# Optimization experiments

Measured on AMD Instinct MI355X. Metric: run time of the kernel, lower is better.

Reference implementation:

```python
import math
import jax, jax.numpy as jnp
import numpy as np

# Module config (init_kwargs)
GRID = (11, 16, 24)          # (T, H, W) latent grid, T odd so T-1 == 2*(T//2)
POOL = 128                   # pool_size / block size
SPARSITY = 0.9
TXT_LEN = 384                # txt_len, txt_first=False
HEADS, HDIM = 8, 128
FFL = GRID[1] * GRID[2]      # first_frame_len = H*W = 384
SEQ = GRID[0] * FFL + TXT_LEN  # 4608 tokens, 36 blocks of 128


def _rearr(t):
    # rearrange_with_remaining, h%8==0 and w%8==0 path.
    # t: [b, (f h w), n, d] with f = T-1 frames (first frame excluded)
    b, s, n, d = t.shape
    T, H, W = GRID
    fn, hn, wn = T // 2, H // 8, W // 8
    x = t.transpose(0, 2, 1, 3).reshape(b * n, fn, 2, hn, 8, wn, 8, d)
    # 'b (fn fb)(hn hb)(wn wb) d -> b (fn hn wn fb hb wb) d'
    x = x.transpose(0, 1, 3, 5, 2, 4, 6, 7).reshape(b * n, s, d)
    return x.reshape(b, n, s, d).transpose(0, 2, 1, 3)


def _inv_rearr(t):
    b, s, n, d = t.shape
    T, H, W = GRID
    fn, hn, wn = T // 2, H // 8, W // 8
    x = t.transpose(0, 2, 1, 3).reshape(b * n, fn, hn, wn, 2, 8, 8, d)
    x = x.transpose(0, 1, 4, 2, 5, 3, 6, 7).reshape(b * n, s, d)
    return x.reshape(b, n, s, d).transpose(0, 2, 1, 3)


def _avgpool(t):
    # seq divisible by POOL -> mean over each block (tail branch unused)
    b, s, n, d = t.shape
    return t.reshape(b, s // POOL, POOL, n, d).mean(axis=2)


def _forward(q, k, v):
    b, s, n, d = q.shape
    scale = jnp.asarray(d, q.dtype) ** -0.5
    # do_tensor_rearrange_pooling on concatenated qkv (txt_first=False)
    qkv = jnp.concatenate([q, k, v], axis=0)
    f_part = qkv[:, :FFL]
    i_part = qkv[:, FFL:s - TXT_LEN]
    t_part = qkv[:, s - TXT_LEN:]
    qkv2 = jnp.concatenate([_rearr(i_part), f_part, t_part], axis=1)
    pool = _avgpool(qkv2)
    q2, k2, v2 = jnp.split(qkv2, 3, axis=0)
    qp, kp, _ = jnp.split(pool, 3, axis=0)
    # pooled block scores + softmax
    ps = jax.nn.softmax(jnp.einsum('blnd,bsnd->bnls', qp, kp) * scale, axis=-1)
    nb = s // POOL
    keep = math.ceil(nb * (1.0 - SPARSITY))
    thr = jax.lax.top_k(ps, keep)[0][..., -1:]
    mask = ps >= thr                              # [B, n, nb, nb] bool
    prot = (FFL + TXT_LEN + POOL - 1) // POOL
    mask = mask.at[:, :, -prot:, :].set(True)
    mask = mask.at[:, :, :, -prot:].set(True)
    bm = mask[0]                                  # [n, nb, nb] per-head block mask (batch 0, as kernel uses)
    tok = jnp.repeat(jnp.repeat(bm, POOL, axis=1), POOL, axis=2)  # [n, S, S]
    # block-sparse attention == masked dense attention over selected kv blocks
    scores = jnp.einsum('bqnd,bknd->bnqk', q2, k2) * scale
    scores = jnp.where(tok[None], scores, jnp.asarray(-1e30, scores.dtype))
    p = jax.nn.softmax(scores, axis=-1)
    x = jnp.einsum('bnqk,bknd->bqnd', p, v2)
    # do_tensor_inv_rearrange (txt_first=False: concat(f, i, t))
    si = s - TXT_LEN - FFL
    xi = _inv_rearr(x[:, :si])
    xf = x[:, si:si + FFL]
    xt = x[:, si + FFL:]
    return jnp.concatenate([xf, xi, xt], axis=1)


def setup_inputs() -> dict:
    key = jax.random.key(0)
    kq, kk, kv = jax.random.split(key, 3)
    q = jax.random.normal(kq, (1, SEQ, HEADS, HDIM), dtype=jnp.float32)
    k = jax.random.normal(kk, (1, SEQ, HEADS, HDIM), dtype=jnp.float32)
    v = jax.random.normal(kv, (1, SEQ, HEADS, HDIM), dtype=jnp.float32)
    t_b_idx = jnp.arange(2, dtype=jnp.int64 if jax.config.jax_enable_x64 else jnp.int32)
    return {'q': q, 'k': k, 'v': v, 't_b_idx': t_b_idx}


def reference(q, k, v, t_b_idx):
    # t_idx = t_b_idx[0] = 0, skip_timesteps = 0 -> sparse branch (static)
    return _forward(q, k, v)
```

## Files before the change

kernel.cpp:

```cpp
#include <hip/hip_runtime.h>


typedef __attribute__((ext_vector_type(8))) _Float16 half8;
typedef __attribute__((ext_vector_type(4))) _Float16 half4;
typedef __attribute__((ext_vector_type(4))) float float4v;

#define KROW 136
#define VROW 72
#define PROW 72

__device__ __forceinline__ int orig_pos(int j) {
    if (j >= 3840) return (j < 4224) ? (j - 3840) : j;
    int blk = j >> 7;
    int r   = j & 127;
    int f   = blk / 6;
    int rem = blk - f * 6;
    int b2  = rem / 3;
    int e   = rem - b2 * 3;
    int a   = r >> 6;
    int c   = (r >> 3) & 7;
    int g   = r & 7;
    return 384 + (f * 2 + a) * 384 + (b2 * 8 + c) * 24 + e * 8 + g;
}

__device__ __forceinline__ void cp16(const void* g, void* l) {
    __builtin_amdgcn_global_load_lds((const __attribute__((address_space(1))) void*)g,
                                     (__attribute__((address_space(3))) void*)l, 16, 0, 0);
}

__global__ __launch_bounds__(256) void prep_kernel(const float* __restrict__ q,
                                                   const float* __restrict__ k,
                                                   const float* __restrict__ v,
                                                   short* __restrict__ Kc,
                                                   unsigned* __restrict__ Vt32,
                                                   float* __restrict__ qp,
                                                   float* __restrict__ kp) {
    __shared__ short Vs[64 * KROW];
    __shared__ float Rs[8 * 128];
    int bx  = blockIdx.x;
    int tid = threadIdx.x;
    int sub = bx & 1;
    int kb  = (bx >> 1) % 36;
    int h   = bx / 72;

    {
        int lr = tid >> 3;
        int ld = (tid & 7) << 2;
#pragma unroll
        for (int pass = 0; pass < 2; ++pass) {
            int lt  = pass * 32 + lr;
            int tok = sub * 64 + lt;
            int op  = orig_pos(kb * 128 + tok);
            const float* kr = k + ((size_t)op * 8 + h) * 128;
            const float* vr = v + ((size_t)op * 8 + h) * 128;
            short* ko = Kc + ((size_t)(h * 36 + kb) * 128 + tok) * KROW;
#pragma unroll
            for (int j = 0; j < 4; ++j) {
                int d = ld + j * 32;
                float4v xk = *reinterpret_cast<const float4v*>(kr + d);
                float4v xv = *reinterpret_cast<const float4v*>(vr + d);
                half4 hk, hv;
#pragma unroll
                for (int i = 0; i < 4; ++i) { hk[i] = (_Float16)xk[i]; hv[i] = (_Float16)xv[i]; }
                *reinterpret_cast<half4*>(ko + d) = hk;
                *reinterpret_cast<half4*>(&Vs[lt * KROW + d]) = hv;
            }
        }
    }

    {
        const float* arr = sub ? q : k;
        int dq = (tid & 31) << 2;
        int g  = tid >> 5;
        float4v acc = {0.f, 0.f, 0.f, 0.f};
        for (int t = g; t < 128; t += 8) {
            int op = orig_pos(kb * 128 + t);
            float4v x = *reinterpret_cast<const float4v*>(arr + ((size_t)op * 8 + h) * 128 + dq);
            acc[0] += x[0]; acc[1] += x[1]; acc[2] += x[2]; acc[3] += x[3];
        }
#pragma unroll
        for (int i = 0; i < 4; ++i) Rs[g * 128 + dq + i] = acc[i];
    }
    __syncthreads();

    {
        const unsigned short* Vsu = (const unsigned short*)Vs;
        unsigned* vo = Vt32 + (size_t)((h * 36 + kb) * 2 + sub) * 128 * (VROW / 2);
#pragma unroll
        for (int it = 0; it < 16; ++it) {
            int i   = it * 256 + tid;
            int tw  = i & 31;
            int dim = i >> 5;
            unsigned lo = Vsu[(2 * tw) * KROW + dim];
            unsigned hi = Vsu[(2 * tw + 1) * KROW + dim];
            vo[dim * (VROW / 2) + tw] = (hi << 16) | lo;
        }
    }

    if (tid < 128) {
        float s = 0.f;
#pragma unroll
        for (int g = 0; g < 8; ++g) s += Rs[g * 128 + tid];
        float* outp = sub ? qp : kp;
        outp[(h * 36 + kb) * 128 + tid] = s * (1.f / 128.f);
    }
}

__global__ __launch_bounds__(256, 3) void flash_kernel(const float* __restrict__ q,
                                                       const short* __restrict__ Kc,
                                                       const short* __restrict__ Vt,
                                                       const float* __restrict__ qp,
                                                       const float* __restrict__ kp,
                                                       float* __restrict__ out,
                                                       float* __restrict__ pO,
                                                       float* __restrict__ pL) {
    __shared__ __align__(16) short Ks[64 * KROW];
    __shared__ __align__(16) short Vsh[128 * VROW];
    __shared__ __align__(16) short Ph[4 * 16 * PROW];
    __shared__ int Ls[40];

    int t = blockIdx.x;
    int h, qb, half, nkb = 0, kbase = 0, pidx = -1;
    if (t < 288) {
        h = t & 7;
        int rest = t >> 3;
        int qbh = rest / 6, r2 = rest % 6;
        half = r2 / 3;
        int chunk = r2 % 3;
        qb = 30 + qbh; nkb = 12; kbase = chunk * 12; pidx = t;
    } else {
        int t2 = t - 288;
        h = t2 & 7;
        int rest = t2 >> 3;
        qb = rest >> 1; half = rest & 1;
    }

    int tid = threadIdx.x, wave = tid >> 6, lane = tid & 63;
    int m16 = lane & 15, quad = lane >> 4;

    int qrow_frag = qb * 128 + half * 64 + wave * 16 + m16;
    const float* qrp = q + ((size_t)orig_pos(qrow_frag) * 8 + h) * 128;
    half8 aq[4];
#pragma unroll
    for (int kc = 0; kc < 4; ++kc) {
        float4v x0 = *reinterpret_cast<const float4v*>(qrp + kc * 32 + quad * 8);
        float4v x1 = *reinterpret_cast<const float4v*>(qrp + kc * 32 + quad * 8 + 4);
#pragma unroll
        for (int j = 0; j < 4; ++j) { aq[kc][j] = (_Float16)x0[j]; aq[kc][4 + j] = (_Float16)x1[j]; }
    }

    if (pidx < 0 && wave == 0) {
        float s = -1e30f;
        if (lane < 36) {
            const float4v* qv = (const float4v*)(qp + (h * 36 + qb) * 128);
            const float4v* kv = (const float4v*)(kp + (h * 36 + lane) * 128);
            float acc = 0.f;
            for (int i = 0; i < 32; ++i) {
                float4v a = qv[i], b = kv[i];
                acc += a[0] * b[0] + a[1] * b[1] + a[2] * b[2] + a[3] * b[3];
            }
            s = acc;
        }
        float tmp = s;
        float thr = 0.f;
        for (int i = 0; i < 4; ++i) {
            float mx = tmp;
            for (int off = 1; off < 64; off <<= 1) mx = fmaxf(mx, __shfl_xor(mx, off));
            thr = mx;
            unsigned long long bal = __ballot(tmp == mx);
            int low = __ffsll(bal) - 1;
            if (lane == low) tmp = -3e38f;
        }
        bool keep = (lane < 36) && ((s >= thr) || (lane >= 30));
        unsigned long long mk = __ballot(keep);
        if (lane == 0) Ls[0] = __popcll(mk);
        if (keep) {
            int pos = __popcll(mk & ((1ull << lane) - 1ull));
            Ls[1 + pos] = lane;
        }
    }
    __syncthreads();
    if (pidx < 0) nkb = Ls[0];

    float l_r[4], o[8][4];
#pragma unroll
    for (int r = 0; r < 4; ++r) l_r[r] = 0.f;
#pragma unroll
    for (int dt = 0; dt < 8; ++dt)
#pragma unroll
        for (int r = 0; r < 4; ++r) o[dt][r] = 0.f;

    constexpr float kScale = 0.08838834764831845f * 1.4426950408889634f;
    short* Phw = Ph + wave * (16 * PROW);

    int ntile = nkb * 2;
    for (int it = 0; it < ntile; ++it) {
        int kb  = (pidx >= 0) ? (kbase + (it >> 1)) : Ls[1 + (it >> 1)];
        int sub = it & 1;
        const char* gK = (const char*)(Kc + ((size_t)((h * 36 + kb) * 128) + sub * 64) * KROW);
        const char* gV = (const char*)(Vt + (size_t)((h * 36 + kb) * 2 + sub) * 128 * VROW);

        __syncthreads();
        {
            char* lK = (char*)Ks;
            char* lV = (char*)Vsh;
            int off = lane * 16;
            for (int c = wave; c < 35; c += 4) {
                if (c < 17) cp16(gK + c * 1024 + off, lK + c * 1024 + off);
                else        cp16(gV + (c - 17) * 1024 + off, lV + (c - 17) * 1024 + off);
            }
        }
        __syncthreads();

        float4v sacc[4];
#pragma unroll
        for (int nt = 0; nt < 4; ++nt) { sacc[nt][0] = 0.f; sacc[nt][1] = 0.f; sacc[nt][2] = 0.f; sacc[nt][3] = 0.f; }
#pragma unroll
        for (int nt = 0; nt < 4; ++nt)
#pragma unroll
            for (int kc = 0; kc < 4; ++kc) {
                half8 bk = *reinterpret_cast<const half8*>(&Ks[(nt * 16 + m16) * KROW + kc * 32 + quad * 8]);
                sacc[nt] = __builtin_amdgcn_mfma_f32_16x16x32_f16(aq[kc], bk, sacc[nt], 0, 0, 0);
            }

#pragma unroll
        for (int r = 0; r < 4; ++r) {
            float p0 = exp2f(sacc[0][r] * kScale);
            float p1 = exp2f(sacc[1][r] * kScale);
            float p2 = exp2f(sacc[2][r] * kScale);
            float p3 = exp2f(sacc[3][r] * kScale);
            sacc[0][r] = p0; sacc[1][r] = p1; sacc[2][r] = p2; sacc[3][r] = p3;
            l_r[r] += (p0 + p1) + (p2 + p3);
        }

#pragma unroll
        for (int nt = 0; nt < 4; ++nt)
#pragma unroll
            for (int r = 0; r < 4; ++r) {
                union { _Float16 hf; short s; } cv;
                cv.hf = (_Float16)sacc[nt][r];
                Phw[(quad * 4 + r) * PROW + nt * 16 + m16] = cv.s;
            }
        half8 ap0 = *reinterpret_cast<const half8*>(&Phw[m16 * PROW + quad * 8]);
        half8 ap1 = *reinterpret_cast<const half8*>(&Phw[m16 * PROW + 32 + quad * 8]);

#pragma unroll
        for (int dt = 0; dt < 8; ++dt) {
            float4v oc;
            oc[0] = o[dt][0]; oc[1] = o[dt][1]; oc[2] = o[dt][2]; oc[3] = o[dt][3];
            half8 bv0 = *reinterpret_cast<const half8*>(&Vsh[(dt * 16 + m16) * VROW + quad * 8]);
            half8 bv1 = *reinterpret_cast<const half8*>(&Vsh[(dt * 16 + m16) * VROW + 32 + quad * 8]);
            oc = __builtin_amdgcn_mfma_f32_16x16x32_f16(ap0, bv0, oc, 0, 0, 0);
            oc = __builtin_amdgcn_mfma_f32_16x16x32_f16(ap1, bv1, oc, 0, 0, 0);
            o[dt][0] = oc[0]; o[dt][1] = oc[1]; o[dt][2] = oc[2]; o[dt][3] = oc[3];
        }
    }

#pragma unroll
    for (int r = 0; r < 4; ++r)
        for (int sh = 1; sh < 16; sh <<= 1) l_r[r] += __shfl_xor(l_r[r], sh);

    if (pidx >= 0) {
        float* po = pO + (size_t)pidx * 8192;
#pragma unroll
        for (int r = 0; r < 4; ++r) {
            int row = wave * 16 + quad * 4 + r;
#pragma unroll
            for (int dt = 0; dt < 8; ++dt)
                po[row * 128 + dt * 16 + m16] = o[dt][r];
            if (m16 == 0) pL[pidx * 64 + row] = l_r[r];
        }
    } else {
#pragma unroll
        for (int r = 0; r < 4; ++r) {
            int qrow = qb * 128 + half * 64 + wave * 16 + quad * 4 + r;
            size_t base = ((size_t)orig_pos(qrow) * 8 + h) * 128;
            float inv = 1.f / l_r[r];
#pragma unroll
            for (int dt = 0; dt < 8; ++dt)
                out[base + dt * 16 + m16] = o[dt][r] * inv;
        }
    }
}

__global__ void combine_kernel(const float* __restrict__ pO, const float* __restrict__ pL,
                               float* __restrict__ out) {
    int g = blockIdx.x;
    int h    = g / 12;
    int rem  = g % 12;
    int qbh  = rem >> 1;
    int half = rem & 1;
    int qb   = 30 + qbh;
    int base_t = (qbh * 6 + half * 3) * 8 + h;

    int tid = threadIdx.x;
    int d   = tid & 127;
    int r0  = tid >> 7;
    for (int itr = 0; itr < 32; ++itr) {
        int row = r0 + itr * 2;
        float l = pL[(base_t + 0) * 64 + row] + pL[(base_t + 8) * 64 + row] + pL[(base_t + 16) * 64 + row];
        float acc = pO[(size_t)(base_t + 0) * 8192 + row * 128 + d]
                  + pO[(size_t)(base_t + 8) * 8192 + row * 128 + d]
                  + pO[(size_t)(base_t + 16) * 8192 + row * 128 + d];
        int qrow = qb * 128 + half * 64 + row;
        out[((size_t)orig_pos(qrow) * 8 + h) * 128 + d] = acc / l;
    }
}

extern "C" void kernel_launch(void* const* d_in, const int* in_sizes, int n_in,
                              void* d_out, int out_size, void* d_ws, size_t ws_size,
                              hipStream_t stream) {
    const float* q = (const float*)d_in[0];
    const float* k = (const float*)d_in[1];
    const float* v = (const float*)d_in[2];
    float* out = (float*)d_out;

    char* w = (char*)d_ws;
    short* Kc  = (short*)(w);
    short* Vt  = (short*)(w + 10027008);
    float* qp  = (float*)(w + 20643840);
    float* kp  = (float*)(w + 20791296);
    float* pL  = (float*)(w + 20938752);
    float* pO  = (float*)(w + 21012480);

    prep_kernel<<<dim3(576), dim3(256), 0, stream>>>(q, k, v, Kc, (unsigned*)Vt, qp, kp);
    flash_kernel<<<dim3(768), dim3(256), 0, stream>>>(q, Kc, Vt, qp, kp, out, pO, pL);
    combine_kernel<<<dim3(96), dim3(256), 0, stream>>>(pO, pL, out);
}
```

Measured before the change: 192.0 us.

## Double-buffer K/V tiles in LDS with async prefetch and parallelize combine

The flash kernel now keeps two LDS buffers for K and V and prefetches the tile two steps ahead with async global-to-LDS copies. Explicit vmcnt waits and barriers replace the old load-then-sync at each step, so tile loads overlap with the MFMA work. The V row pitch shrinks to 68 so the doubled buffers fit, MFMA sections get raised wave priority, and launch bounds drop to two blocks per CU. The combine kernel is split across eight times as many blocks. The costs are lower occupancy, V rows that are no longer 16-byte aligned, which may split LDS vector reads, and a redundant duplicate K-chunk copy added to keep the vmcnt counts uniform across waves.

```diff
diff --git a/kernel.cpp b/kernel.cpp
--- a/kernel.cpp
+++ b/kernel.cpp
@@ -6,7 +6,7 @@
 typedef __attribute__((ext_vector_type(4))) float float4v;
 
 #define KROW 136
-#define VROW 72
+#define VROW 68
 #define PROW 72
 
 __device__ __forceinline__ int orig_pos(int j) {
@@ -106,7 +106,22 @@
     }
 }
 
-__global__ __launch_bounds__(256, 3) void flash_kernel(const float* __restrict__ q,
+__device__ __forceinline__ void stage_tile(const short* __restrict__ Kc,
+                                           const short* __restrict__ Vt,
+                                           int h, int kb, int sub,
+                                           int wave, int lane,
+                                           char* lK, char* lV) {
+    const char* gK = (const char*)(Kc + ((size_t)((h * 36 + kb) * 128) + sub * 64) * KROW);
+    const char* gV = (const char*)(Vt + (size_t)((h * 36 + kb) * 2 + sub) * 128 * VROW);
+    int off = lane * 16;
+    for (int c = wave; c < 34; c += 4) {
+        if (c < 17) cp16(gK + c * 1024 + off, lK + c * 1024 + off);
+        else        cp16(gV + (c - 17) * 1024 + off, lV + (c - 17) * 1024 + off);
+    }
+    if (wave >= 2) cp16(gK + wave * 1024 + off, lK + wave * 1024 + off);
+}
+
+__global__ __launch_bounds__(256, 2) void flash_kernel(const float* __restrict__ q,
                                                        const short* __restrict__ Kc,
                                                        const short* __restrict__ Vt,
                                                        const float* __restrict__ qp,
@@ -114,8 +129,8 @@
                                                        float* __restrict__ out,
                                                        float* __restrict__ pO,
                                                        float* __restrict__ pL) {
-    __shared__ __align__(16) short Ks[64 * KROW];
-    __shared__ __align__(16) short Vsh[128 * VROW];
+    __shared__ __align__(16) short Ks[2][64 * KROW];
+    __shared__ __align__(16) short Vsh[2][128 * VROW];
     __shared__ __align__(16) short Ph[4 * 16 * PROW];
     __shared__ int Ls[40];
 
@@ -194,34 +209,32 @@
     short* Phw = Ph + wave * (16 * PROW);
 
     int ntile = nkb * 2;
+
+    {
+        int kb0 = (pidx >= 0) ? kbase : Ls[1];
+        stage_tile(Kc, Vt, h, kb0, 0, wave, lane, (char*)&Ks[0][0], (char*)&Vsh[0][0]);
+        stage_tile(Kc, Vt, h, kb0, 1, wave, lane, (char*)&Ks[1][0], (char*)&Vsh[1][0]);
+    }
+
     for (int it = 0; it < ntile; ++it) {
-        int kb  = (pidx >= 0) ? (kbase + (it >> 1)) : Ls[1 + (it >> 1)];
-        int sub = it & 1;
-        const char* gK = (const char*)(Kc + ((size_t)((h * 36 + kb) * 128) + sub * 64) * KROW);
-        const char* gV = (const char*)(Vt + (size_t)((h * 36 + kb) * 2 + sub) * 128 * VROW);
-
-        __syncthreads();
-        {
-            char* lK = (char*)Ks;
-            char* lV = (char*)Vsh;
-            int off = lane * 16;
-            for (int c = wave; c < 35; c += 4) {
-                if (c < 17) cp16(gK + c * 1024 + off, lK + c * 1024 + off);
-                else        cp16(gV + (c - 17) * 1024 + off, lV + (c - 17) * 1024 + off);
-            }
-        }
-        __syncthreads();
+        int cur = it & 1;
+        if (it + 1 < ntile) { asm volatile("s_waitcnt vmcnt(9)" ::: "memory"); }
+        else                { asm volatile("s_waitcnt vmcnt(0)" ::: "memory"); }
+        __builtin_amdgcn_s_barrier();
+        __builtin_amdgcn_sched_barrier(0);
 
         float4v sacc[4];
 #pragma unroll
         for (int nt = 0; nt < 4; ++nt) { sacc[nt][0] = 0.f; sacc[nt][1] = 0.f; sacc[nt][2] = 0.f; sacc[nt][3] = 0.f; }
+        __builtin_amdgcn_s_setprio(1);
 #pragma unroll
         for (int nt = 0; nt < 4; ++nt)
 #pragma unroll
             for (int kc = 0; kc < 4; ++kc) {
-                half8 bk = *reinterpret_cast<const half8*>(&Ks[(nt * 16 + m16) * KROW + kc * 32 + quad * 8]);
+                half8 bk = *reinterpret_cast<const half8*>(&Ks[cur][(nt * 16 + m16) * KROW + kc * 32 + quad * 8]);
                 sacc[nt] = __builtin_amdgcn_mfma_f32_16x16x32_f16(aq[kc], bk, sacc[nt], 0, 0, 0);
             }
+        __builtin_amdgcn_s_setprio(0);
 
 #pragma unroll
         for (int r = 0; r < 4; ++r) {
@@ -244,15 +257,25 @@
         half8 ap0 = *reinterpret_cast<const half8*>(&Phw[m16 * PROW + quad * 8]);
         half8 ap1 = *reinterpret_cast<const half8*>(&Phw[m16 * PROW + 32 + quad * 8]);
 
+        __builtin_amdgcn_s_setprio(1);
 #pragma unroll
         for (int dt = 0; dt < 8; ++dt) {
             float4v oc;
             oc[0] = o[dt][0]; oc[1] = o[dt][1]; oc[2] = o[dt][2]; oc[3] = o[dt][3];
-            half8 bv0 = *reinterpret_cast<const half8*>(&Vsh[(dt * 16 + m16) * VROW + quad * 8]);
-            half8 bv1 = *reinterpret_cast<const half8*>(&Vsh[(dt * 16 + m16) * VROW + 32 + quad * 8]);
+            half8 bv0 = *reinterpret_cast<const half8*>(&Vsh[cur][(dt * 16 + m16) * VROW + quad * 8]);
+            half8 bv1 = *reinterpret_cast<const half8*>(&Vsh[cur][(dt * 16 + m16) * VROW + 32 + quad * 8]);
             oc = __builtin_amdgcn_mfma_f32_16x16x32_f16(ap0, bv0, oc, 0, 0, 0);
             oc = __builtin_amdgcn_mfma_f32_16x16x32_f16(ap1, bv1, oc, 0, 0, 0);
             o[dt][0] = oc[0]; o[dt][1] = oc[1]; o[dt][2] = oc[2]; o[dt][3] = oc[3];
+        }
+        __builtin_amdgcn_s_setprio(0);
+
+        __builtin_amdgcn_sched_barrier(0);
+        __builtin_amdgcn_s_barrier();
+        if (it + 2 < ntile) {
+            int it2 = it + 2;
+            int kb2 = (pidx >= 0) ? (kbase + (it2 >> 1)) : Ls[1 + (it2 >> 1)];
+            stage_tile(Kc, Vt, h, kb2, it2 & 1, wave, lane, (char*)&Ks[cur][0], (char*)&Vsh[cur][0]);
         }
     }
 
@@ -285,7 +308,9 @@
 
 __global__ void combine_kernel(const float* __restrict__ pO, const float* __restrict__ pL,
                                float* __restrict__ out) {
-    int g = blockIdx.x;
+    int gb = blockIdx.x;
+    int g  = gb >> 3;
+    int rg = gb & 7;
     int h    = g / 12;
     int rem  = g % 12;
     int qbh  = rem >> 1;
@@ -296,8 +321,9 @@
     int tid = threadIdx.x;
     int d   = tid & 127;
     int r0  = tid >> 7;
-    for (int itr = 0; itr < 32; ++itr) {
-        int row = r0 + itr * 2;
+#pragma unroll
+    for (int itr = 0; itr < 4; ++itr) {
+        int row = rg * 8 + r0 + itr * 2;
         float l = pL[(base_t + 0) * 64 + row] + pL[(base_t + 8) * 64 + row] + pL[(base_t + 16) * 64 + row];
         float acc = pO[(size_t)(base_t + 0) * 8192 + row * 128 + d]
                   + pO[(size_t)(base_t + 8) * 8192 + row * 128 + d]
@@ -318,12 +344,12 @@
     char* w = (char*)d_ws;
     short* Kc  = (short*)(w);
     short* Vt  = (short*)(w + 10027008);
-    float* qp  = (float*)(w + 20643840);
-    float* kp  = (float*)(w + 20791296);
-    float* pL  = (float*)(w + 20938752);
-    float* pO  = (float*)(w + 21012480);
+    float* qp  = (float*)(w + 20054016);
+    float* kp  = (float*)(w + 20201472);
+    float* pL  = (float*)(w + 20348928);
+    float* pO  = (float*)(w + 20422656);
 
     prep_kernel<<<dim3(576), dim3(256), 0, stream>>>(q, k, v, Kc, (unsigned*)Vt, qp, kp);
     flash_kernel<<<dim3(768), dim3(256), 0, stream>>>(q, Kc, Vt, qp, kp, out, pO, pL);
-    combine_kernel<<<dim3(96), dim3(256), 0, stream>>>(pO, pL, out);
-}
+    combine_kernel<<<dim3(768), dim3(256), 0, stream>>>(pO, pL, out);
+}
```

New measurement: 217.7 us. 1.13x slower.

## Give each flash wave 32 query rows, split prep kernel, widen combine grid

Applied to the files above, without the earlier changes.

The flash kernel now runs 2 waves of 128 threads, each owning 32 query rows (two 16-row groups). Each K/V fragment loaded from LDS therefore feeds two MFMAs, halving LDS reads per MFMA. The softmax scale is folded into Q at load time, and the V and P LDS row padding shrinks from 72 to 68. The prep kernel is split into separate blocks for K/V conversion and for pooling, and the combine kernel uses 8 times more blocks, both to add parallelism. In exchange the flash kernel roughly doubles its accumulator registers and has fewer waves per block for latency hiding; the new padding may also change LDS bank conflicts.

```diff
diff --git a/kernel.cpp b/kernel.cpp
--- a/kernel.cpp
+++ b/kernel.cpp
@@ -6,8 +6,8 @@
 typedef __attribute__((ext_vector_type(4))) float float4v;
 
 #define KROW 136
-#define VROW 72
-#define PROW 72
+#define VROW 68
+#define PPROW 68
 
 __device__ __forceinline__ int orig_pos(int j) {
     if (j >= 3840) return (j < 4224) ? (j - 3840) : j;
@@ -39,11 +39,12 @@
     __shared__ float Rs[8 * 128];
     int bx  = blockIdx.x;
     int tid = threadIdx.x;
-    int sub = bx & 1;
-    int kb  = (bx >> 1) % 36;
-    int h   = bx / 72;
-
-    {
+
+    if (bx < 576) {
+        int sub = bx & 1;
+        int kb  = (bx >> 1) % 36;
+        int h   = bx / 72;
+
         int lr = tid >> 3;
         int ld = (tid & 7) << 2;
 #pragma unroll
@@ -66,47 +67,53 @@
                 *reinterpret_cast<half4*>(&Vs[lt * KROW + d]) = hv;
             }
         }
-    }
-
-    {
+        __syncthreads();
+
+        {
+            const unsigned short* Vsu = (const unsigned short*)Vs;
+            unsigned* vo = Vt32 + (size_t)((h * 36 + kb) * 2 + sub) * 128 * (VROW / 2);
+#pragma unroll
+            for (int it = 0; it < 16; ++it) {
+                int i   = it * 256 + tid;
+                int tw  = i & 31;
+                int dim = i >> 5;
+                unsigned lo = Vsu[(2 * tw) * KROW + dim];
+                unsigned hi = Vsu[(2 * tw + 1) * KROW + dim];
+                vo[dim * (VROW / 2) + tw] = (hi << 16) | lo;
+            }
+        }
+    } else {
+        int bx2 = bx - 576;
+        int sub = bx2 & 1;
+        int kb  = (bx2 >> 1) % 36;
+        int h   = bx2 / 72;
+
         const float* arr = sub ? q : k;
         int dq = (tid & 31) << 2;
         int g  = tid >> 5;
         float4v acc = {0.f, 0.f, 0.f, 0.f};
-        for (int t = g; t < 128; t += 8) {
+#pragma unroll
+        for (int it = 0; it < 16; ++it) {
+            int t  = g + it * 8;
             int op = orig_pos(kb * 128 + t);
             float4v x = *reinterpret_cast<const float4v*>(arr + ((size_t)op * 8 + h) * 128 + dq);
             acc[0] += x[0]; acc[1] += x[1]; acc[2] += x[2]; acc[3] += x[3];
         }
 #pragma unroll
         for (int i = 0; i < 4; ++i) Rs[g * 128 + dq + i] = acc[i];
-    }
-    __syncthreads();
-
-    {
-        const unsigned short* Vsu = (const unsigned short*)Vs;
-        unsigned* vo = Vt32 + (size_t)((h * 36 + kb) * 2 + sub) * 128 * (VROW / 2);
-#pragma unroll
-        for (int it = 0; it < 16; ++it) {
-            int i   = it * 256 + tid;
-            int tw  = i & 31;
-            int dim = i >> 5;
-            unsigned lo = Vsu[(2 * tw) * KROW + dim];
-            unsigned hi = Vsu[(2 * tw + 1) * KROW + dim];
-            vo[dim * (VROW / 2) + tw] = (hi << 16) | lo;
-        }
-    }
-
-    if (tid < 128) {
-        float s = 0.f;
-#pragma unroll
-        for (int g = 0; g < 8; ++g) s += Rs[g * 128 + tid];
-        float* outp = sub ? qp : kp;
-        outp[(h * 36 + kb) * 128 + tid] = s * (1.f / 128.f);
-    }
-}
-
-__global__ __launch_bounds__(256, 3) void flash_kernel(const float* __restrict__ q,
+        __syncthreads();
+
+        if (tid < 128) {
+            float s = 0.f;
+#pragma unroll
+            for (int g2 = 0; g2 < 8; ++g2) s += Rs[g2 * 128 + tid];
+            float* outp = sub ? qp : kp;
+            outp[(h * 36 + kb) * 128 + tid] = s * (1.f / 128.f);
+        }
+    }
+}
+
+__global__ __launch_bounds__(128, 2) void flash_kernel(const float* __restrict__ q,
                                                        const short* __restrict__ Kc,
                                                        const short* __restrict__ Vt,
                                                        const float* __restrict__ qp,
@@ -116,7 +123,7 @@
                                                        float* __restrict__ pL) {
     __shared__ __align__(16) short Ks[64 * KROW];
     __shared__ __align__(16) short Vsh[128 * VROW];
-    __shared__ __align__(16) short Ph[4 * 16 * PROW];
+    __shared__ __align__(16) short Ph[2 * 32 * PPROW];
     __shared__ int Ls[40];
 
     int t = blockIdx.x;
@@ -138,15 +145,23 @@
     int tid = threadIdx.x, wave = tid >> 6, lane = tid & 63;
     int m16 = lane & 15, quad = lane >> 4;
 
-    int qrow_frag = qb * 128 + half * 64 + wave * 16 + m16;
-    const float* qrp = q + ((size_t)orig_pos(qrow_frag) * 8 + h) * 128;
-    half8 aq[4];
-#pragma unroll
-    for (int kc = 0; kc < 4; ++kc) {
-        float4v x0 = *reinterpret_cast<const float4v*>(qrp + kc * 32 + quad * 8);
-        float4v x1 = *reinterpret_cast<const float4v*>(qrp + kc * 32 + quad * 8 + 4);
-#pragma unroll
-        for (int j = 0; j < 4; ++j) { aq[kc][j] = (_Float16)x0[j]; aq[kc][4 + j] = (_Float16)x1[j]; }
+    constexpr float kScale = 0.08838834764831845f * 1.4426950408889634f;
+
+    half8 aq[2][4];
+#pragma unroll
+    for (int rg = 0; rg < 2; ++rg) {
+        int qrow_frag = qb * 128 + half * 64 + wave * 32 + rg * 16 + m16;
+        const float* qrp = q + ((size_t)orig_pos(qrow_frag) * 8 + h) * 128;
+#pragma unroll
+        for (int kc = 0; kc < 4; ++kc) {
+            float4v x0 = *reinterpret_cast<const float4v*>(qrp + kc * 32 + quad * 8);
+            float4v x1 = *reinterpret_cast<const float4v*>(qrp + kc * 32 + quad * 8 + 4);
+#pragma unroll
+            for (int j = 0; j < 4; ++j) {
+                aq[rg][kc][j]     = (_Float16)(x0[j] * kScale);
+                aq[rg][kc][4 + j] = (_Float16)(x1[j] * kScale);
+            }
+        }
     }
 
     if (pidx < 0 && wave == 0) {
@@ -182,16 +197,17 @@
     __syncthreads();
     if (pidx < 0) nkb = Ls[0];
 
-    float l_r[4], o[8][4];
-#pragma unroll
-    for (int r = 0; r < 4; ++r) l_r[r] = 0.f;
-#pragma unroll
-    for (int dt = 0; dt < 8; ++dt)
-#pragma unroll
-        for (int r = 0; r < 4; ++r) o[dt][r] = 0.f;
-
-    constexpr float kScale = 0.08838834764831845f * 1.4426950408889634f;
-    short* Phw = Ph + wave * (16 * PROW);
+    float l_r[2][4];
+    float4v o[2][8];
+#pragma unroll
+    for (int rg = 0; rg < 2; ++rg) {
+#pragma unroll
+        for (int r = 0; r < 4; ++r) l_r[rg][r] = 0.f;
+#pragma unroll
+        for (int dt = 0; dt < 8; ++dt) { o[rg][dt][0] = 0.f; o[rg][dt][1] = 0.f; o[rg][dt][2] = 0.f; o[rg][dt][3] = 0.f; }
+    }
+
+    short* Phw = Ph + wave * (32 * PPROW);
 
     int ntile = nkb * 2;
     for (int it = 0; it < ntile; ++it) {
@@ -205,87 +221,108 @@
             char* lK = (char*)Ks;
             char* lV = (char*)Vsh;
             int off = lane * 16;
-            for (int c = wave; c < 35; c += 4) {
+            for (int c = wave; c < 34; c += 2) {
                 if (c < 17) cp16(gK + c * 1024 + off, lK + c * 1024 + off);
                 else        cp16(gV + (c - 17) * 1024 + off, lV + (c - 17) * 1024 + off);
             }
         }
         __syncthreads();
 
-        float4v sacc[4];
-#pragma unroll
-        for (int nt = 0; nt < 4; ++nt) { sacc[nt][0] = 0.f; sacc[nt][1] = 0.f; sacc[nt][2] = 0.f; sacc[nt][3] = 0.f; }
+        float4v sacc[2][4];
+#pragma unroll
+        for (int rg = 0; rg < 2; ++rg)
+#pragma unroll
+            for (int nt = 0; nt < 4; ++nt) { sacc[rg][nt][0] = 0.f; sacc[rg][nt][1] = 0.f; sacc[rg][nt][2] = 0.f; sacc[rg][nt][3] = 0.f; }
 #pragma unroll
         for (int nt = 0; nt < 4; ++nt)
 #pragma unroll
             for (int kc = 0; kc < 4; ++kc) {
                 half8 bk = *reinterpret_cast<const half8*>(&Ks[(nt * 16 + m16) * KROW + kc * 32 + quad * 8]);
-                sacc[nt] = __builtin_amdgcn_mfma_f32_16x16x32_f16(aq[kc], bk, sacc[nt], 0, 0, 0);
-            }
-
-#pragma unroll
-        for (int r = 0; r < 4; ++r) {
-            float p0 = exp2f(sacc[0][r] * kScale);
-            float p1 = exp2f(sacc[1][r] * kScale);
-            float p2 = exp2f(sacc[2][r] * kScale);
-            float p3 = exp2f(sacc[3][r] * kScale);
-            sacc[0][r] = p0; sacc[1][r] = p1; sacc[2][r] = p2; sacc[3][r] = p3;
-            l_r[r] += (p0 + p1) + (p2 + p3);
-        }
-
-#pragma unroll
-        for (int nt = 0; nt < 4; ++nt)
+                sacc[0][nt] = __builtin_amdgcn_mfma_f32_16x16x32_f16(aq[0][kc], bk, sacc[0][nt], 0, 0, 0);
+                sacc[1][nt] = __builtin_amdgcn_mfma_f32_16x16x32_f16(aq[1][kc], bk, sacc[1][nt], 0, 0, 0);
+            }
+
+#pragma unroll
+        for (int rg = 0; rg < 2; ++rg)
 #pragma unroll
             for (int r = 0; r < 4; ++r) {
-                union { _Float16 hf; short s; } cv;
-                cv.hf = (_Float16)sacc[nt][r];
-                Phw[(quad * 4 + r) * PROW + nt * 16 + m16] = cv.s;
-            }
-        half8 ap0 = *reinterpret_cast<const half8*>(&Phw[m16 * PROW + quad * 8]);
-        half8 ap1 = *reinterpret_cast<const half8*>(&Phw[m16 * PROW + 32 + quad * 8]);
+                float p0 = exp2f(sacc[rg][0][r]);
+                float p1 = exp2f(sacc[rg][1][r]);
+                float p2 = exp2f(sacc[rg][2][r]);
+                float p3 = exp2f(sacc[rg][3][r]);
+                sacc[rg][0][r] = p0; sacc[rg][1][r] = p1; sacc[rg][2][r] = p2; sacc[rg][3][r] = p3;
+                l_r[rg][r] += (p0 + p1) + (p2 + p3);
+            }
+
+#pragma unroll
+        for (int rg = 0; rg < 2; ++rg)
+#pragma unroll
+            for (int nt = 0; nt < 4; ++nt)
+#pragma unroll
+                for (int r = 0; r < 4; ++r) {
+                    union { _Float16 hf; short s; } cv;
+                    cv.hf = (_Float16)sacc[rg][nt][r];
+                    Phw[(rg * 16 + quad * 4 + r) * PPROW + nt * 16 + m16] = cv.s;
+                }
+        half8 ap[2][2];
+#pragma unroll
+        for (int rg = 0; rg < 2; ++rg) {
+            ap[rg][0] = *reinterpret_cast<const half8*>(&Phw[(rg * 16 + m16) * PPROW + quad * 8]);
+            ap[rg][1] = *reinterpret_cast<const half8*>(&Phw[(rg * 16 + m16) * PPROW + 32 + quad * 8]);
+        }
 
 #pragma unroll
         for (int dt = 0; dt < 8; ++dt) {
-            float4v oc;
-            oc[0] = o[dt][0]; oc[1] = o[dt][1]; oc[2] = o[dt][2]; oc[3] = o[dt][3];
             half8 bv0 = *reinterpret_cast<const half8*>(&Vsh[(dt * 16 + m16) * VROW + quad * 8]);
             half8 bv1 = *reinterpret_cast<const half8*>(&Vsh[(dt * 16 + m16) * VROW + 32 + quad * 8]);
-            oc = __builtin_amdgcn_mfma_f32_16x16x32_f16(ap0, bv0, oc, 0, 0, 0);
-            oc = __builtin_amdgcn_mfma_f32_16x16x32_f16(ap1, bv1, oc, 0, 0, 0);
-            o[dt][0] = oc[0]; o[dt][1] = oc[1]; o[dt][2] = oc[2]; o[dt][3] = oc[3];
-        }
-    }
-
-#pragma unroll
-    for (int r = 0; r < 4; ++r)
-        for (int sh = 1; sh < 16; sh <<= 1) l_r[r] += __shfl_xor(l_r[r], sh);
+#pragma unroll
+            for (int rg = 0; rg < 2; ++rg) {
+                float4v oc = o[rg][dt];
+                oc = __builtin_amdgcn_mfma_f32_16x16x32_f16(ap[rg][0], bv0, oc, 0, 0, 0);
+                oc = __builtin_amdgcn_mfma_f32_16x16x32_f16(ap[rg][1], bv1, oc, 0, 0, 0);
+                o[rg][dt] = oc;
+            }
+        }
+    }
+
+#pragma unroll
+    for (int rg = 0; rg < 2; ++rg)
+#pragma unroll
+        for (int r = 0; r < 4; ++r)
+            for (int sh = 1; sh < 16; sh <<= 1) l_r[rg][r] += __shfl_xor(l_r[rg][r], sh);
 
     if (pidx >= 0) {
         float* po = pO + (size_t)pidx * 8192;
 #pragma unroll
-        for (int r = 0; r < 4; ++r) {
-            int row = wave * 16 + quad * 4 + r;
-#pragma unroll
-            for (int dt = 0; dt < 8; ++dt)
-                po[row * 128 + dt * 16 + m16] = o[dt][r];
-            if (m16 == 0) pL[pidx * 64 + row] = l_r[r];
-        }
+        for (int rg = 0; rg < 2; ++rg)
+#pragma unroll
+            for (int r = 0; r < 4; ++r) {
+                int row = wave * 32 + rg * 16 + quad * 4 + r;
+#pragma unroll
+                for (int dt = 0; dt < 8; ++dt)
+                    po[row * 128 + dt * 16 + m16] = o[rg][dt][r];
+                if (m16 == 0) pL[pidx * 64 + row] = l_r[rg][r];
+            }
     } else {
 #pragma unroll
-        for (int r = 0; r < 4; ++r) {
-            int qrow = qb * 128 + half * 64 + wave * 16 + quad * 4 + r;
-            size_t base = ((size_t)orig_pos(qrow) * 8 + h) * 128;
-            float inv = 1.f / l_r[r];
-#pragma unroll
-            for (int dt = 0; dt < 8; ++dt)
-                out[base + dt * 16 + m16] = o[dt][r] * inv;
-        }
+        for (int rg = 0; rg < 2; ++rg)
+#pragma unroll
+            for (int r = 0; r < 4; ++r) {
+                int qrow = qb * 128 + half * 64 + wave * 32 + rg * 16 + quad * 4 + r;
+                size_t base = ((size_t)orig_pos(qrow) * 8 + h) * 128;
+                float inv = 1.f / l_r[rg][r];
+#pragma unroll
+                for (int dt = 0; dt < 8; ++dt)
+                    out[base + dt * 16 + m16] = o[rg][dt][r] * inv;
+            }
     }
 }
 
 __global__ void combine_kernel(const float* __restrict__ pO, const float* __restrict__ pL,
                                float* __restrict__ out) {
-    int g = blockIdx.x;
+    int gb = blockIdx.x;
+    int g  = gb >> 3;
+    int rg = gb & 7;
     int h    = g / 12;
     int rem  = g % 12;
     int qbh  = rem >> 1;
@@ -296,8 +333,9 @@
     int tid = threadIdx.x;
     int d   = tid & 127;
     int r0  = tid >> 7;
-    for (int itr = 0; itr < 32; ++itr) {
-        int row = r0 + itr * 2;
+#pragma unroll
+    for (int itr = 0; itr < 4; ++itr) {
+        int row = rg * 8 + r0 + itr * 2;
         float l = pL[(base_t + 0) * 64 + row] + pL[(base_t + 8) * 64 + row] + pL[(base_t + 16) * 64 + row];
         float acc = pO[(size_t)(base_t + 0) * 8192 + row * 128 + d]
                   + pO[(size_t)(base_t + 8) * 8192 + row * 128 + d]
@@ -318,12 +356,12 @@
     char* w = (char*)d_ws;
     short* Kc  = (short*)(w);
     short* Vt  = (short*)(w + 10027008);
-    float* qp  = (float*)(w + 20643840);
-    float* kp  = (float*)(w + 20791296);
-    float* pL  = (float*)(w + 20938752);
-    float* pO  = (float*)(w + 21012480);
-
-    prep_kernel<<<dim3(576), dim3(256), 0, stream>>>(q, k, v, Kc, (unsigned*)Vt, qp, kp);
-    flash_kernel<<<dim3(768), dim3(256), 0, stream>>>(q, Kc, Vt, qp, kp, out, pO, pL);
-    combine_kernel<<<dim3(96), dim3(256), 0, stream>>>(pO, pL, out);
-}
+    float* qp  = (float*)(w + 20054016);
+    float* kp  = (float*)(w + 20201472);
+    float* pL  = (float*)(w + 20348928);
+    float* pO  = (float*)(w + 20422656);
+
+    prep_kernel<<<dim3(1152), dim3(256), 0, stream>>>(q, k, v, Kc, (unsigned*)Vt, qp, kp);
+    flash_kernel<<<dim3(768), dim3(128), 0, stream>>>(q, Kc, Vt, qp, kp, out, pO, pL);
+    combine_kernel<<<dim3(768), dim3(256), 0, stream>>>(pO, pL, out);
+}
```

New measurement: 196.4 us. +2.3%, slower.
